# Performance work log

Measured on AMD Instinct MI355X. Metric: run time of the kernel, lower is better.

## Reference

```python
import jax, jax.numpy as jnp
import numpy as np

C = 32
C_Z = 128
S = 256
N_SEQ = 256
LN_EPS = 1e-5


def setup_inputs() -> dict:
    key = jax.random.key(0)
    k1, k2, k3, k4 = jax.random.split(key, 4)
    m_si = jax.random.normal(k1, (S, N_SEQ, C), dtype=jnp.float32)
    ln_gamma = jnp.ones((C,), dtype=jnp.float32)
    ln_beta = jnp.zeros((C,), dtype=jnp.float32)
    # nn.Linear(c, 2c, bias=False): weight shape (2c, c)
    W_ab = jax.random.normal(k2, (2 * C, C), dtype=jnp.float32) / np.sqrt(C)
    # nn.Linear(c*c, c_z): weight (c_z, c*c), bias (c_z,)
    W_out = jax.random.normal(k3, (C_Z, C * C), dtype=jnp.float32) / np.sqrt(C * C)
    b_out = jax.random.normal(k4, (C_Z,), dtype=jnp.float32) * 0.01
    return {"m_si": m_si, "ln_gamma": ln_gamma, "ln_beta": ln_beta,
            "W_ab": W_ab, "W_out": W_out, "b_out": b_out}


def reference(m_si, ln_gamma, ln_beta, W_ab, W_out, b_out):
    # LayerNorm over channel dim c
    mu = jnp.mean(m_si, axis=-1, keepdims=True)
    var = jnp.var(m_si, axis=-1, keepdims=True)
    x = (m_si - mu) * jax.lax.rsqrt(var + LN_EPS) * ln_gamma + ln_beta
    # linear_no_bias then chunk into a, b: each (s, n_seq, c)
    ab = jnp.einsum('snc,dc->snd', x, W_ab)
    a, b = ab[..., :C], ab[..., C:]
    # mean over MSA sequences of outer products a[s,i,:] x b[s,j,:]
    # restructured as a contraction over n_seq: (i, j, c, c)
    outer = jnp.einsum('inc,jnd->ijcd', a, b) / N_SEQ
    outer = outer.reshape(S, S, C * C)  # flatten (c, c) -> c*c
    # final linear projection to c_z
    z_ij = jnp.einsum('ijk,zk->ijz', outer, W_out) + b_out
    return z_ij
```

## Files before the change

### kernel.cpp

```cpp
#include <hip/hip_runtime.h>

#define SDIM 256
#define NSEQ 256
#define CDIM 32
#define CZ 128
#define IB 8
#define JB 4

typedef __bf16 bfx8 __attribute__((ext_vector_type(8)));
typedef float fx4 __attribute__((ext_vector_type(4)));
typedef float f32x16 __attribute__((ext_vector_type(16)));
typedef unsigned int u32x4 __attribute__((ext_vector_type(4)));

__device__ __forceinline__ unsigned short f2bf(float f) {
  unsigned int u = __float_as_uint(f);
  u += 0x7fffu + ((u >> 16) & 1u);
  return (unsigned short)(u >> 16);
}

__device__ __forceinline__ unsigned int cvtpk(float lo, float hi) {
  unsigned int r;
  asm("v_cvt_pk_bf16_f32 %0, %1, %2" : "=v"(r) : "v"(lo), "v"(hi));
  return r;
}

__device__ __forceinline__ void gload16(const void* g, void* l) {
  __builtin_amdgcn_global_load_lds((const __attribute__((address_space(1))) unsigned int*)g,
                                   (__attribute__((address_space(3))) unsigned int*)l,
                                   16, 0, 0);
}


__global__ __launch_bounds__(256) void opm_prep(
    const float* __restrict__ m_si, const float* __restrict__ gamma, const float* __restrict__ beta,
    const float* __restrict__ Wab, const float* __restrict__ Wout,
    unsigned short* __restrict__ a_t, unsigned short* __restrict__ b_t,
    unsigned short* __restrict__ w2T)
{
  __shared__ __align__(16) char shbuf[41216];
  const int b = blockIdx.x;
  const int t = threadIdx.x;
  if (b < 2 * SDIM) {
    float* xin = (float*)shbuf;
    unsigned short* xt = (unsigned short*)shbuf;
    fx4* wab4 = (fx4*)(shbuf + 36864);
    float* gbuf = (float*)(shbuf + 36864 + 4096);
    const int s = b >> 1, dph = b & 1;

    const float* msrc = m_si + s * 8192;
#pragma unroll
    for (int k = 0; k < 8; ++k) {
      const int q = t + k * 256;
      ((fx4*)xin)[(q >> 3) * 9 + (q & 7)] = ((const fx4*)msrc)[q];
    }
    wab4[t & 255] = ((const fx4*)(Wab + dph * 1024))[t & 255];
    if (t < 32) { gbuf[t] = gamma[t]; gbuf[32 + t] = beta[t]; }
    __syncthreads();

    float x[CDIM];
#pragma unroll
    for (int c = 0; c < CDIM; ++c) x[c] = xin[t * 36 + c];
    __syncthreads();

    float mu = 0.f;
#pragma unroll
    for (int c = 0; c < CDIM; ++c) mu += x[c];
    mu *= (1.f / CDIM);
    float var = 0.f;
#pragma unroll
    for (int c = 0; c < CDIM; ++c) { float d = x[c] - mu; var += d * d; }
    var *= (1.f / CDIM);
    const float inv = rsqrtf(var + 1e-5f);
    fx4 xv[8];
#pragma unroll
    for (int cq = 0; cq < 8; ++cq) {
      fx4 v;
#pragma unroll
      for (int j = 0; j < 4; ++j) {
        const int c = cq * 4 + j;
        v[j] = (x[c] - mu) * inv * gbuf[c] + gbuf[32 + c];
      }
      xv[cq] = v;
    }

    for (int dp = 0; dp < 32; ++dp) {
      fx4 a = xv[0] * wab4[dp * 8];
#pragma unroll
      for (int cq = 1; cq < 8; ++cq) a += xv[cq] * wab4[dp * 8 + cq];
      xt[dp * 256 + t] = f2bf(a[0] + a[1] + a[2] + a[3]);
    }
    __syncthreads();

    unsigned short* outb = dph ? b_t : a_t;
#pragma unroll
    for (int k = 0; k < 4; ++k) {
      const int q = t + k * 256;
      const int row = q >> 5, cc = q & 31;
      *(u32x4*)(outb + (s * 32 + row) * 256 + cc * 8) = *(const u32x4*)(shbuf + row * 512 + cc * 16);
    }
  } else {
    unsigned short* lin = (unsigned short*)shbuf;
    const int blk = b - 2 * SDIM;
    const float* wsrc = Wout + blk * 16384;
#pragma unroll
    for (int jj = 0; jj < 16; ++jj) {
      const int q = t + jj * 256;
      const fx4 v = ((const fx4*)wsrc)[q];
      unsigned short* dst = lin + q * 4;
      dst[0] = f2bf(v[0]); dst[1] = f2bf(v[1]); dst[2] = f2bf(v[2]); dst[3] = f2bf(v[3]);
    }
    __syncthreads();
    const int zt = blk >> 1;
    const int zlbase = (blk & 1) * 16;
#pragma unroll
    for (int w = 0; w < 8; ++w) {
      const int id = t + w * 256;
      const int zll = id & 15;
      const int h  = (id >> 4) & 1;
      const int ks = id >> 5;
      unsigned short vals[8];
#pragma unroll
      for (int e = 0; e < 8; ++e) {
        const int kp = ks * 16 + h * 8 + e;
        const int c = (kp & 3) | (((kp >> 8) & 1) << 2) | (((kp >> 2) & 1) << 3) | (((kp >> 9) & 1) << 4);
        const int d = (kp >> 3) & 31;
        vals[e] = lin[zll * 1024 + c * CDIM + d];
      }
      const int dest = (zt << 15) + (ks << 9) + (h << 8) + ((zlbase + zll) << 3);
      *(u32x4*)(w2T + dest) = *(const u32x4*)vals;
    }
  }
}

__global__ __launch_bounds__(512, 4) void opm_main(
    const unsigned short* __restrict__ a_t, const unsigned short* __restrict__ b_t,
    const unsigned short* __restrict__ w2T, const float* __restrict__ bout,
    float* __restrict__ out)
{
  __shared__ __align__(16) char smem[65536];
  char* o_sh = smem;

  const int tid = threadIdx.x;
  const int lane = tid & 63;
  const int wid = tid >> 6;
  const int l31 = lane & 31;
  const int h = lane >> 5;

  const int bxr = blockIdx.x;
  const int bx = (bxr & 7) * 256 + (bxr >> 3);
  const int i0 = (bx >> 6) * IB;
  const int j0 = (bx & 63) * JB;

  const int wm = wid >> 1;
  const int wn = wid & 1;
  const int wbase = wid * 1024;

  f32x16 acc00 = {}, acc01 = {}, acc10 = {}, acc11 = {};

  auto STAGE = [&](int buf, int nc) {
    const int nbase = nc * 32;
    char* A = smem + 16384 + buf * 16384;
    char* B = smem + 49152 + buf * 8192;
#pragma unroll
    for (int pass = 0; pass < 2; ++pass) {
      const int q = pass * 512 + tid;
      const int row = q >> 2;
      const int gs = (q & 3) ^ ((q >> 3) & 3);
      const unsigned short* src = a_t + ((i0 + (row >> 5)) * 32 + (row & 31)) * 256 + nbase + gs * 8;
      gload16(src, A + pass * 8192 + wbase);
    }
    {
      const int q = tid;
      const int row = q >> 2;
      const int gs = (q & 3) ^ ((q >> 3) & 3);
      const unsigned short* src = b_t + ((j0 + (row >> 5)) * 32 + (row & 31)) * 256 + nbase + gs * 8;
      gload16(src, B + wbase);
    }
  };

  auto COMPUTE = [&](int buf) {
    char* A = smem + 16384 + buf * 16384;
    char* B = smem + 49152 + buf * 8192;
#pragma unroll
    for (int ks = 0; ks < 2; ++ks) {
      const int s = ks * 2 + h;
      bfx8 af0, af1, bf0, bf1;
      { const int r = wm * 64 + l31;      af0 = *(const bfx8*)(A + r * 64 + (((s ^ (r >> 1)) & 3) << 4)); }
      { const int r = wm * 64 + 32 + l31; af1 = *(const bfx8*)(A + r * 64 + (((s ^ (r >> 1)) & 3) << 4)); }
      { const int r = wn * 64 + l31;      bf0 = *(const bfx8*)(B + r * 64 + (((s ^ (r >> 1)) & 3) << 4)); }
      { const int r = wn * 64 + 32 + l31; bf1 = *(const bfx8*)(B + r * 64 + (((s ^ (r >> 1)) & 3) << 4)); }
      __builtin_amdgcn_s_setprio(1);
      acc00 = __builtin_amdgcn_mfma_f32_32x32x16_bf16(af0, bf0, acc00, 0, 0, 0);
      acc01 = __builtin_amdgcn_mfma_f32_32x32x16_bf16(af0, bf1, acc01, 0, 0, 0);
      acc10 = __builtin_amdgcn_mfma_f32_32x32x16_bf16(af1, bf0, acc10, 0, 0, 0);
      acc11 = __builtin_amdgcn_mfma_f32_32x32x16_bf16(af1, bf1, acc11, 0, 0, 0);
      __builtin_amdgcn_s_setprio(0);
    }
  };

  STAGE(0, 0);
#pragma unroll 2
  for (int t = 0; t < 8; ++t) {
    if (t < 7) {
      STAGE((t + 1) & 1, t + 1);
      asm volatile("s_waitcnt vmcnt(3)" ::: "memory");
    } else {
      asm volatile("s_waitcnt vmcnt(0)" ::: "memory");
    }
    __builtin_amdgcn_s_barrier();
    asm volatile("" ::: "memory");
    COMPUTE(t & 1);
    asm volatile("s_waitcnt lgkmcnt(0)" ::: "memory");
    __builtin_amdgcn_s_barrier();
  }

  {
    const f32x16 av[4] = { acc00 * 0.00390625f, acc01 * 0.00390625f,
                           acc10 * 0.00390625f, acc11 * 0.00390625f };
#pragma unroll
    for (int mi = 0; mi < 2; ++mi) {
#pragma unroll
      for (int ni = 0; ni < 2; ++ni) {
        const f32x16 a = av[mi * 2 + ni];
        const int p = (wm * 2 + mi) * 4 + (wn * 2 + ni);
#pragma unroll
        for (int c4 = 0; c4 < 2; ++c4) {
          const int sl = l31 + 32 * h + 64 * c4;
          u32x4 v;
          v[0] = cvtpk(a[8 * c4 + 0], a[8 * c4 + 1]);
          v[1] = cvtpk(a[8 * c4 + 2], a[8 * c4 + 3]);
          v[2] = cvtpk(a[8 * c4 + 4], a[8 * c4 + 5]);
          v[3] = cvtpk(a[8 * c4 + 6], a[8 * c4 + 7]);
          *(u32x4*)(o_sh + p * 2048 + ((sl ^ (p & 7)) << 4)) = v;
        }
      }
    }
  }
  __syncthreads();

  {
    const int zt = wid & 3;
    const int kh = wid >> 2;
    const unsigned short* wp = w2T + (zt << 15) + (h << 8) + (l31 << 3);
    const int obase = l31 * 2048;
    const int oxor = (l31 & 7) << 4;
    bfx8 wfv[4], ofv[2];
#pragma unroll
    for (int pf = 0; pf < 4; ++pf) wfv[pf] = *(const bfx8*)(wp + ((kh * 32 + pf) << 9));
#pragma unroll
    for (int pf = 0; pf < 2; ++pf) {
      const int sl = 2 * (kh * 32 + pf) + h;
      ofv[pf] = *(const bfx8*)(o_sh + obase + ((sl << 4) ^ oxor));
    }
    f32x16 accB = {};
#pragma unroll
    for (int k = 0; k < 32; ++k) {
      __builtin_amdgcn_s_setprio(1);
      accB = __builtin_amdgcn_mfma_f32_32x32x16_bf16(wfv[k & 3], ofv[k & 1], accB, 0, 0, 0);
      __builtin_amdgcn_s_setprio(0);
      if (k + 4 < 32) wfv[k & 3] = *(const bfx8*)(wp + ((kh * 32 + k + 4) << 9));
      if (k + 2 < 32) {
        const int sl = 2 * (kh * 32 + k + 2) + h;
        ofv[k & 1] = *(const bfx8*)(o_sh + obase + ((sl << 4) ^ oxor));
      }
    }
    __syncthreads();

#pragma unroll
    for (int g2 = 0; g2 < 4; ++g2) {
      fx4 v = { accB[4 * g2], accB[4 * g2 + 1], accB[4 * g2 + 2], accB[4 * g2 + 3] };
      const int s = g2 * 2 + h;
      *(fx4*)(o_sh + kh * 16384 + zt * 4096 + ((s * 32 + l31) << 4)) = v;
    }
  }
  __syncthreads();

#pragma unroll
  for (int k = 0; k < 2; ++k) {
    const int v = tid + k * 512;
    const int zt2 = v >> 8, s2 = (v >> 5) & 7, pp = v & 31;
    const int off = zt2 * 4096 + ((s2 * 32 + pp) << 4);
    fx4 r = *(fx4*)(o_sh + off) + *(fx4*)(o_sh + 16384 + off);
    const int z0 = zt2 * 32 + s2 * 4;
    r += *(const fx4*)(bout + z0);
    const int i = i0 + (pp >> 2), j = j0 + (pp & 3);
    __builtin_nontemporal_store(r, (fx4*)(out + (i * SDIM + j) * CZ + z0));
  }
}

extern "C" void kernel_launch(void* const* d_in, const int* in_sizes, int n_in,
                              void* d_out, int out_size, void* d_ws, size_t ws_size,
                              hipStream_t stream) {
  const float* m_si  = (const float*)d_in[0];
  const float* gamma = (const float*)d_in[1];
  const float* beta  = (const float*)d_in[2];
  const float* Wab   = (const float*)d_in[3];
  const float* Wout  = (const float*)d_in[4];
  const float* bout  = (const float*)d_in[5];
  float* out = (float*)d_out;

  char* ws = (char*)d_ws;
  unsigned short* a_t = (unsigned short*)ws;
  unsigned short* b_t = (unsigned short*)(ws + (4u << 20));
  unsigned short* w2T = (unsigned short*)(ws + (8u << 20));

  opm_prep<<<dim3(2 * SDIM + 8), dim3(256), 0, stream>>>(m_si, gamma, beta, Wab, Wout, a_t, b_t, w2T);
  opm_main<<<dim3(2048), dim3(512), 0, stream>>>(a_t, b_t, w2T, bout, out);
}
```

Baseline: 85.85 us.

## Restructure output projection split, tree-reduce partials, remap block order, spread W prep

The W_out prep now uses 32 smaller blocks instead of 8, so each block transposes 4 output channels rather than 16. In the main kernel each wave computes two z-tiles over a quarter of K, reusing each loaded operand fragment for two MFMAs. The partial sums are combined with a two-level LDS tree reduction, and the output is written with plain stores instead of nontemporal ones. The block-to-tile mapping now groups 16x16 tile regions per XCD for better L2 locality, at the cost of more synchronisation steps in the reduction.

```diff
diff --git a/kernel.cpp b/kernel.cpp
--- a/kernel.cpp
+++ b/kernel.cpp
@@ -101,32 +101,32 @@
   } else {
     unsigned short* lin = (unsigned short*)shbuf;
     const int blk = b - 2 * SDIM;
-    const float* wsrc = Wout + blk * 16384;
-#pragma unroll
-    for (int jj = 0; jj < 16; ++jj) {
+    const float* wsrc = Wout + blk * 4096;
+#pragma unroll
+    for (int jj = 0; jj < 4; ++jj) {
       const int q = t + jj * 256;
       const fx4 v = ((const fx4*)wsrc)[q];
       unsigned short* dst = lin + q * 4;
       dst[0] = f2bf(v[0]); dst[1] = f2bf(v[1]); dst[2] = f2bf(v[2]); dst[3] = f2bf(v[3]);
     }
     __syncthreads();
-    const int zt = blk >> 1;
-    const int zlbase = (blk & 1) * 16;
-#pragma unroll
-    for (int w = 0; w < 8; ++w) {
+    const int z0 = blk * 4;
+#pragma unroll
+    for (int w = 0; w < 2; ++w) {
       const int id = t + w * 256;
-      const int zll = id & 15;
-      const int h  = (id >> 4) & 1;
-      const int ks = id >> 5;
+      const int lz = id & 3;
+      const int hh = (id >> 2) & 1;
+      const int ks = id >> 3;
+      const int z = z0 + lz;
       unsigned short vals[8];
 #pragma unroll
       for (int e = 0; e < 8; ++e) {
-        const int kp = ks * 16 + h * 8 + e;
+        const int kp = ks * 16 + hh * 8 + e;
         const int c = (kp & 3) | (((kp >> 8) & 1) << 2) | (((kp >> 2) & 1) << 3) | (((kp >> 9) & 1) << 4);
         const int d = (kp >> 3) & 31;
-        vals[e] = lin[zll * 1024 + c * CDIM + d];
-      }
-      const int dest = (zt << 15) + (ks << 9) + (h << 8) + ((zlbase + zll) << 3);
+        vals[e] = lin[lz * 1024 + c * CDIM + d];
+      }
+      const int dest = ((z >> 5) << 15) + (ks << 9) + (hh << 8) + ((z & 31) << 3);
       *(u32x4*)(w2T + dest) = *(const u32x4*)vals;
     }
   }
@@ -147,9 +147,12 @@
   const int h = lane >> 5;
 
   const int bxr = blockIdx.x;
-  const int bx = (bxr & 7) * 256 + (bxr >> 3);
-  const int i0 = (bx >> 6) * IB;
-  const int j0 = (bx & 63) * JB;
+  const int xc = bxr & 7;
+  const int q8 = bxr >> 3;
+  const int it = q8 >> 4;
+  const int jt = q8 & 15;
+  const int i0 = ((xc & 1) * 16 + it) * IB;
+  const int j0 = ((xc >> 1) * 16 + jt) * JB;
 
   const int wm = wid >> 1;
   const int wn = wid & 1;
@@ -239,52 +242,88 @@
   __syncthreads();
 
   {
-    const int zt = wid & 3;
-    const int kh = wid >> 2;
-    const unsigned short* wp = w2T + (zt << 15) + (h << 8) + (l31 << 3);
+    const int ztp = wid & 1;
+    const int kh = wid >> 1;
+    const unsigned short* wpa = w2T + ((ztp * 2 + 0) << 15) + (h << 8) + (l31 << 3);
+    const unsigned short* wpb = w2T + ((ztp * 2 + 1) << 15) + (h << 8) + (l31 << 3);
     const int obase = l31 * 2048;
-    const int oxor = (l31 & 7) << 4;
-    bfx8 wfv[4], ofv[2];
-#pragma unroll
-    for (int pf = 0; pf < 4; ++pf) wfv[pf] = *(const bfx8*)(wp + ((kh * 32 + pf) << 9));
-#pragma unroll
-    for (int pf = 0; pf < 2; ++pf) {
-      const int sl = 2 * (kh * 32 + pf) + h;
-      ofv[pf] = *(const bfx8*)(o_sh + obase + ((sl << 4) ^ oxor));
-    }
-    f32x16 accB = {};
-#pragma unroll
-    for (int k = 0; k < 32; ++k) {
+    const int oxor = l31 & 7;
+    const int ks0 = kh * 16;
+
+    bfx8 wa[4], wb[4];
+#pragma unroll
+    for (int q = 0; q < 4; ++q) {
+      wa[q] = *(const bfx8*)(wpa + ((ks0 + q) << 9));
+      wb[q] = *(const bfx8*)(wpb + ((ks0 + q) << 9));
+    }
+    bfx8 oc = *(const bfx8*)(o_sh + obase + ((((ks0 << 1) + h) ^ oxor) << 4));
+    bfx8 on = *(const bfx8*)(o_sh + obase + (((((ks0 + 1) << 1) + h) ^ oxor) << 4));
+
+    f32x16 za = {}, zb = {};
+#pragma unroll
+    for (int st = 0; st < 16; ++st) {
+      const int q = st & 3;
       __builtin_amdgcn_s_setprio(1);
-      accB = __builtin_amdgcn_mfma_f32_32x32x16_bf16(wfv[k & 3], ofv[k & 1], accB, 0, 0, 0);
+      za = __builtin_amdgcn_mfma_f32_32x32x16_bf16(wa[q], oc, za, 0, 0, 0);
+      zb = __builtin_amdgcn_mfma_f32_32x32x16_bf16(wb[q], oc, zb, 0, 0, 0);
       __builtin_amdgcn_s_setprio(0);
-      if (k + 4 < 32) wfv[k & 3] = *(const bfx8*)(wp + ((kh * 32 + k + 4) << 9));
-      if (k + 2 < 32) {
-        const int sl = 2 * (kh * 32 + k + 2) + h;
-        ofv[k & 1] = *(const bfx8*)(o_sh + obase + ((sl << 4) ^ oxor));
-      }
-    }
-    __syncthreads();
-
-#pragma unroll
-    for (int g2 = 0; g2 < 4; ++g2) {
-      fx4 v = { accB[4 * g2], accB[4 * g2 + 1], accB[4 * g2 + 2], accB[4 * g2 + 3] };
-      const int s = g2 * 2 + h;
-      *(fx4*)(o_sh + kh * 16384 + zt * 4096 + ((s * 32 + l31) << 4)) = v;
-    }
-  }
-  __syncthreads();
-
-#pragma unroll
-  for (int k = 0; k < 2; ++k) {
-    const int v = tid + k * 512;
-    const int zt2 = v >> 8, s2 = (v >> 5) & 7, pp = v & 31;
-    const int off = zt2 * 4096 + ((s2 * 32 + pp) << 4);
-    fx4 r = *(fx4*)(o_sh + off) + *(fx4*)(o_sh + 16384 + off);
-    const int z0 = zt2 * 32 + s2 * 4;
-    r += *(const fx4*)(bout + z0);
-    const int i = i0 + (pp >> 2), j = j0 + (pp & 3);
-    __builtin_nontemporal_store(r, (fx4*)(out + (i * SDIM + j) * CZ + z0));
+      oc = on;
+      if (st < 14) on = *(const bfx8*)(o_sh + obase + (((((ks0 + st + 2) << 1) + h) ^ oxor) << 4));
+      if (st < 12) {
+        wa[q] = *(const bfx8*)(wpa + ((ks0 + st + 4) << 9));
+        wb[q] = *(const bfx8*)(wpb + ((ks0 + st + 4) << 9));
+      }
+    }
+    __syncthreads();
+
+    const int slot = (kh >> 1) * 2 + ztp;
+    auto PWRITE = [&](char* base) {
+#pragma unroll
+      for (int zs = 0; zs < 2; ++zs) {
+        const f32x16& A = zs ? zb : za;
+#pragma unroll
+        for (int g2 = 0; g2 < 4; ++g2) {
+          fx4 v = { A[4 * g2], A[4 * g2 + 1], A[4 * g2 + 2], A[4 * g2 + 3] };
+          *(fx4*)(base + zs * 4096 + (((g2 * 2 + h) * 32 + l31) << 4)) = v;
+        }
+      }
+    };
+    auto PADD = [&](const char* base) {
+#pragma unroll
+      for (int zs = 0; zs < 2; ++zs) {
+        f32x16& A = zs ? zb : za;
+#pragma unroll
+        for (int g2 = 0; g2 < 4; ++g2) {
+          const fx4 v = *(const fx4*)(base + zs * 4096 + (((g2 * 2 + h) * 32 + l31) << 4));
+          A[4 * g2 + 0] += v[0]; A[4 * g2 + 1] += v[1];
+          A[4 * g2 + 2] += v[2]; A[4 * g2 + 3] += v[3];
+        }
+      }
+    };
+    if (kh & 1) PWRITE(o_sh + slot * 8192);
+    __syncthreads();
+    if (!(kh & 1)) {
+      PADD(o_sh + slot * 8192);
+      if (kh == 2) PWRITE(o_sh + 32768 + ztp * 8192);
+    }
+    __syncthreads();
+    if (kh == 0) {
+      PADD(o_sh + 32768 + ztp * 8192);
+      const int i = i0 + (l31 >> 2), j = j0 + (l31 & 3);
+      float* op = out + (i * SDIM + j) * CZ + ztp * 64;
+      const float* bp = bout + ztp * 64;
+#pragma unroll
+      for (int zs = 0; zs < 2; ++zs) {
+        const f32x16& A = zs ? zb : za;
+#pragma unroll
+        for (int g2 = 0; g2 < 4; ++g2) {
+          const int zl = zs * 32 + g2 * 8 + h * 4;
+          fx4 v = { A[4 * g2], A[4 * g2 + 1], A[4 * g2 + 2], A[4 * g2 + 3] };
+          v += *(const fx4*)(bp + zl);
+          *(fx4*)(op + zl) = v;
+        }
+      }
+    }
   }
 }
 
@@ -304,6 +343,6 @@
   unsigned short* b_t = (unsigned short*)(ws + (4u << 20));
   unsigned short* w2T = (unsigned short*)(ws + (8u << 20));
 
-  opm_prep<<<dim3(2 * SDIM + 8), dim3(256), 0, stream>>>(m_si, gamma, beta, Wab, Wout, a_t, b_t, w2T);
+  opm_prep<<<dim3(2 * SDIM + 32), dim3(256), 0, stream>>>(m_si, gamma, beta, Wab, Wout, a_t, b_t, w2T);
   opm_main<<<dim3(2048), dim3(512), 0, stream>>>(a_t, b_t, w2T, bout, out);
 }
```

After: 81.41 us. -5.2%, faster.

## Halve output tile to 4x4 pairs, 256-thread blocks, 16x16 MFMA projection

Applied to the files above, without the earlier changes.

Shrinks each main-kernel block from an 8x4 to a 4x4 (i,j) tile with 256 threads and 32KB LDS, doubling the grid to 4096 blocks. The second GEMM (outer product times W_out) now uses 16x16x32 MFMAs with a new W_out layout built in the prep kernel, and a two-way k-split reduced through LDS. The block-to-tile mapping is rearranged for L2 locality. The aim is higher occupancy and a better fit of the projection GEMM to the smaller tile, at the cost of less A-operand reuse per block and more W_out traffic per output.

```diff
diff --git a/kernel.cpp b/kernel.cpp
--- a/kernel.cpp
+++ b/kernel.cpp
@@ -4,7 +4,7 @@
 #define NSEQ 256
 #define CDIM 32
 #define CZ 128
-#define IB 8
+#define IB 4
 #define JB 4
 
 typedef __bf16 bfx8 __attribute__((ext_vector_type(8)));
@@ -101,43 +101,44 @@
   } else {
     unsigned short* lin = (unsigned short*)shbuf;
     const int blk = b - 2 * SDIM;
-    const float* wsrc = Wout + blk * 16384;
-#pragma unroll
-    for (int jj = 0; jj < 16; ++jj) {
+    const float* wsrc = Wout + blk * 4096;
+#pragma unroll
+    for (int jj = 0; jj < 4; ++jj) {
       const int q = t + jj * 256;
       const fx4 v = ((const fx4*)wsrc)[q];
       unsigned short* dst = lin + q * 4;
       dst[0] = f2bf(v[0]); dst[1] = f2bf(v[1]); dst[2] = f2bf(v[2]); dst[3] = f2bf(v[3]);
     }
     __syncthreads();
-    const int zt = blk >> 1;
-    const int zlbase = (blk & 1) * 16;
-#pragma unroll
-    for (int w = 0; w < 8; ++w) {
+    const int z0 = blk * 4;
+#pragma unroll
+    for (int w = 0; w < 2; ++w) {
       const int id = t + w * 256;
-      const int zll = id & 15;
-      const int h  = (id >> 4) & 1;
-      const int ks = id >> 5;
+      const int lz = id & 3;
+      const int rest = id >> 2;
+      const int g = rest & 3;
+      const int ksg = rest >> 2;
+      const int z = z0 + lz;
       unsigned short vals[8];
 #pragma unroll
       for (int e = 0; e < 8; ++e) {
-        const int kp = ks * 16 + h * 8 + e;
+        const int kp = ksg * 32 + g * 8 + e;
         const int c = (kp & 3) | (((kp >> 8) & 1) << 2) | (((kp >> 2) & 1) << 3) | (((kp >> 9) & 1) << 4);
         const int d = (kp >> 3) & 31;
-        vals[e] = lin[zll * 1024 + c * CDIM + d];
+        vals[e] = lin[lz * 1024 + c * CDIM + d];
       }
-      const int dest = (zt << 15) + (ks << 9) + (h << 8) + ((zlbase + zll) << 3);
+      const int dest = ((z >> 4) * 32 + ksg) * 512 + g * 128 + (z & 15) * 8;
       *(u32x4*)(w2T + dest) = *(const u32x4*)vals;
     }
   }
 }
 
-__global__ __launch_bounds__(512, 4) void opm_main(
+__global__ __launch_bounds__(256, 4) void opm_main(
     const unsigned short* __restrict__ a_t, const unsigned short* __restrict__ b_t,
     const unsigned short* __restrict__ w2T, const float* __restrict__ bout,
     float* __restrict__ out)
 {
-  __shared__ __align__(16) char smem[65536];
+  __shared__ __align__(16) char smem[32768];
   char* o_sh = smem;
 
   const int tid = threadIdx.x;
@@ -147,9 +148,12 @@
   const int h = lane >> 5;
 
   const int bxr = blockIdx.x;
-  const int bx = (bxr & 7) * 256 + (bxr >> 3);
-  const int i0 = (bx >> 6) * IB;
-  const int j0 = (bx & 63) * JB;
+  const int xc = bxr & 7;
+  const int q9 = bxr >> 3;
+  const int it = (xc & 1) * 32 + (q9 >> 4);
+  const int jt = (xc >> 1) * 16 + (q9 & 15);
+  const int i0 = it * IB;
+  const int j0 = jt * JB;
 
   const int wm = wid >> 1;
   const int wn = wid & 1;
@@ -159,28 +163,29 @@
 
   auto STAGE = [&](int buf, int nc) {
     const int nbase = nc * 32;
-    char* A = smem + 16384 + buf * 16384;
-    char* B = smem + 49152 + buf * 8192;
+    char* A = smem + buf * 8192;
+    char* B = smem + 16384 + buf * 8192;
 #pragma unroll
     for (int pass = 0; pass < 2; ++pass) {
-      const int q = pass * 512 + tid;
+      const int q = pass * 256 + tid;
       const int row = q >> 2;
       const int gs = (q & 3) ^ ((q >> 3) & 3);
-      const unsigned short* src = a_t + ((i0 + (row >> 5)) * 32 + (row & 31)) * 256 + nbase + gs * 8;
-      gload16(src, A + pass * 8192 + wbase);
-    }
-    {
-      const int q = tid;
+      const unsigned short* src = a_t + (i0 * 32 + row) * 256 + nbase + gs * 8;
+      gload16(src, A + pass * 4096 + wbase);
+    }
+#pragma unroll
+    for (int pass = 0; pass < 2; ++pass) {
+      const int q = pass * 256 + tid;
       const int row = q >> 2;
       const int gs = (q & 3) ^ ((q >> 3) & 3);
-      const unsigned short* src = b_t + ((j0 + (row >> 5)) * 32 + (row & 31)) * 256 + nbase + gs * 8;
-      gload16(src, B + wbase);
+      const unsigned short* src = b_t + (j0 * 32 + row) * 256 + nbase + gs * 8;
+      gload16(src, B + pass * 4096 + wbase);
     }
   };
 
   auto COMPUTE = [&](int buf) {
-    char* A = smem + 16384 + buf * 16384;
-    char* B = smem + 49152 + buf * 8192;
+    char* A = smem + buf * 8192;
+    char* B = smem + 16384 + buf * 8192;
 #pragma unroll
     for (int ks = 0; ks < 2; ++ks) {
       const int s = ks * 2 + h;
@@ -203,7 +208,7 @@
   for (int t = 0; t < 8; ++t) {
     if (t < 7) {
       STAGE((t + 1) & 1, t + 1);
-      asm volatile("s_waitcnt vmcnt(3)" ::: "memory");
+      asm volatile("s_waitcnt vmcnt(4)" ::: "memory");
     } else {
       asm volatile("s_waitcnt vmcnt(0)" ::: "memory");
     }
@@ -239,52 +244,67 @@
   __syncthreads();
 
   {
-    const int zt = wid & 3;
-    const int kh = wid >> 2;
-    const unsigned short* wp = w2T + (zt << 15) + (h << 8) + (l31 << 3);
-    const int obase = l31 * 2048;
-    const int oxor = (l31 & 7) << 4;
-    bfx8 wfv[4], ofv[2];
-#pragma unroll
-    for (int pf = 0; pf < 4; ++pf) wfv[pf] = *(const bfx8*)(wp + ((kh * 32 + pf) << 9));
-#pragma unroll
-    for (int pf = 0; pf < 2; ++pf) {
-      const int sl = 2 * (kh * 32 + pf) + h;
-      ofv[pf] = *(const bfx8*)(o_sh + obase + ((sl << 4) ^ oxor));
-    }
-    f32x16 accB = {};
-#pragma unroll
-    for (int k = 0; k < 32; ++k) {
+    const int ztp = wid & 1;
+    const int kh = wid >> 1;
+    const int zb = ztp * 4;
+    const unsigned short* wq = w2T + lane * 8;
+    const int p = lane & 15;
+    const int g = lane >> 4;
+    const int obase = p * 2048;
+    const int oxor = p & 7;
+    const int ks0 = kh * 16;
+
+    bfx8 wA0 = *(const bfx8*)(wq + ((zb + 0) * 32 + ks0) * 512);
+    bfx8 wA1 = *(const bfx8*)(wq + ((zb + 1) * 32 + ks0) * 512);
+    bfx8 wA2 = *(const bfx8*)(wq + ((zb + 2) * 32 + ks0) * 512);
+    bfx8 wA3 = *(const bfx8*)(wq + ((zb + 3) * 32 + ks0) * 512);
+    bfx8 oA = *(const bfx8*)(o_sh + obase + ((((ks0 * 4 + g)) ^ oxor) << 4));
+
+    fx4 az0 = {0.f,0.f,0.f,0.f}, az1 = {0.f,0.f,0.f,0.f};
+    fx4 az2 = {0.f,0.f,0.f,0.f}, az3 = {0.f,0.f,0.f,0.f};
+#pragma unroll
+    for (int st = 0; st < 16; ++st) {
+      bfx8 wB0, wB1, wB2, wB3, oB;
+      if (st < 15) {
+        const int nk = ks0 + st + 1;
+        wB0 = *(const bfx8*)(wq + ((zb + 0) * 32 + nk) * 512);
+        wB1 = *(const bfx8*)(wq + ((zb + 1) * 32 + nk) * 512);
+        wB2 = *(const bfx8*)(wq + ((zb + 2) * 32 + nk) * 512);
+        wB3 = *(const bfx8*)(wq + ((zb + 3) * 32 + nk) * 512);
+        oB = *(const bfx8*)(o_sh + obase + (((nk * 4 + g) ^ oxor) << 4));
+      }
       __builtin_amdgcn_s_setprio(1);
-      accB = __builtin_amdgcn_mfma_f32_32x32x16_bf16(wfv[k & 3], ofv[k & 1], accB, 0, 0, 0);
+      az0 = __builtin_amdgcn_mfma_f32_16x16x32_bf16(wA0, oA, az0, 0, 0, 0);
+      az1 = __builtin_amdgcn_mfma_f32_16x16x32_bf16(wA1, oA, az1, 0, 0, 0);
+      az2 = __builtin_amdgcn_mfma_f32_16x16x32_bf16(wA2, oA, az2, 0, 0, 0);
+      az3 = __builtin_amdgcn_mfma_f32_16x16x32_bf16(wA3, oA, az3, 0, 0, 0);
       __builtin_amdgcn_s_setprio(0);
-      if (k + 4 < 32) wfv[k & 3] = *(const bfx8*)(wp + ((kh * 32 + k + 4) << 9));
-      if (k + 2 < 32) {
-        const int sl = 2 * (kh * 32 + k + 2) + h;
-        ofv[k & 1] = *(const bfx8*)(o_sh + obase + ((sl << 4) ^ oxor));
-      }
-    }
-    __syncthreads();
-
-#pragma unroll
-    for (int g2 = 0; g2 < 4; ++g2) {
-      fx4 v = { accB[4 * g2], accB[4 * g2 + 1], accB[4 * g2 + 2], accB[4 * g2 + 3] };
-      const int s = g2 * 2 + h;
-      *(fx4*)(o_sh + kh * 16384 + zt * 4096 + ((s * 32 + l31) << 4)) = v;
-    }
-  }
-  __syncthreads();
-
-#pragma unroll
-  for (int k = 0; k < 2; ++k) {
-    const int v = tid + k * 512;
-    const int zt2 = v >> 8, s2 = (v >> 5) & 7, pp = v & 31;
-    const int off = zt2 * 4096 + ((s2 * 32 + pp) << 4);
-    fx4 r = *(fx4*)(o_sh + off) + *(fx4*)(o_sh + 16384 + off);
-    const int z0 = zt2 * 32 + s2 * 4;
-    r += *(const fx4*)(bout + z0);
-    const int i = i0 + (pp >> 2), j = j0 + (pp & 3);
-    __builtin_nontemporal_store(r, (fx4*)(out + (i * SDIM + j) * CZ + z0));
+      if (st < 15) { wA0 = wB0; wA1 = wB1; wA2 = wB2; wA3 = wB3; oA = oB; }
+    }
+    __syncthreads();
+
+    char* pb = smem + ztp * 4096;
+    if (kh == 1) {
+      *(fx4*)(pb + 0 * 1024 + lane * 16) = az0;
+      *(fx4*)(pb + 1 * 1024 + lane * 16) = az1;
+      *(fx4*)(pb + 2 * 1024 + lane * 16) = az2;
+      *(fx4*)(pb + 3 * 1024 + lane * 16) = az3;
+    }
+    __syncthreads();
+    if (kh == 0) {
+      az0 += *(const fx4*)(pb + 0 * 1024 + lane * 16);
+      az1 += *(const fx4*)(pb + 1 * 1024 + lane * 16);
+      az2 += *(const fx4*)(pb + 2 * 1024 + lane * 16);
+      az3 += *(const fx4*)(pb + 3 * 1024 + lane * 16);
+      const int i = i0 + (p >> 2), j = j0 + (p & 3);
+      float* op = out + (i * SDIM + j) * CZ;
+      const int zq = g * 4;
+      fx4 v;
+      v = az0 + *(const fx4*)(bout + (zb + 0) * 16 + zq); *(fx4*)(op + (zb + 0) * 16 + zq) = v;
+      v = az1 + *(const fx4*)(bout + (zb + 1) * 16 + zq); *(fx4*)(op + (zb + 1) * 16 + zq) = v;
+      v = az2 + *(const fx4*)(bout + (zb + 2) * 16 + zq); *(fx4*)(op + (zb + 2) * 16 + zq) = v;
+      v = az3 + *(const fx4*)(bout + (zb + 3) * 16 + zq); *(fx4*)(op + (zb + 3) * 16 + zq) = v;
+    }
   }
 }
 
@@ -304,6 +324,6 @@
   unsigned short* b_t = (unsigned short*)(ws + (4u << 20));
   unsigned short* w2T = (unsigned short*)(ws + (8u << 20));
 
-  opm_prep<<<dim3(2 * SDIM + 8), dim3(256), 0, stream>>>(m_si, gamma, beta, Wab, Wout, a_t, b_t, w2T);
-  opm_main<<<dim3(2048), dim3(512), 0, stream>>>(a_t, b_t, w2T, bout, out);
-}
+  opm_prep<<<dim3(2 * SDIM + 32), dim3(256), 0, stream>>>(m_si, gamma, beta, Wab, Wout, a_t, b_t, w2T);
+  opm_main<<<dim3(4096), dim3(256), 0, stream>>>(a_t, b_t, w2T, bout, out);
+}
```

After: 93.22 us. +8.6%, slower.
